# Kernel optimization log

Measured on AMD Instinct MI355X. Metric: run time of the kernel, lower is better.

Reference implementation:

```python
import jax, jax.numpy as jnp
import numpy as np

DIM = 2048
NUM_HEADS = 16
HEAD_DIM = DIM // NUM_HEADS
SCALE = 1.0 / float(np.sqrt(HEAD_DIM))


def setup_inputs() -> dict:
    key = jax.random.key(0)
    ks = jax.random.split(key, 7)
    B, L = 2, 2048
    x = jax.random.normal(ks[0], (B, L, DIM), dtype=jnp.float32)
    s = 1.0 / np.sqrt(DIM)
    # nn.Linear stores weight as [out, in]; y = x @ W.T + b
    Wq = jax.random.uniform(ks[1], (DIM, DIM), jnp.float32, -s, s)
    bq = jax.random.uniform(ks[2], (DIM,), jnp.float32, -s, s)
    Wk = jax.random.uniform(ks[3], (DIM, DIM), jnp.float32, -s, s)
    bk = jax.random.uniform(ks[4], (DIM,), jnp.float32, -s, s)
    Wv = jax.random.uniform(ks[5], (DIM, DIM), jnp.float32, -s, s)
    bv = jax.random.uniform(ks[6], (DIM,), jnp.float32, -s, s)
    return {"x": x, "Wq": Wq, "bq": bq, "Wk": Wk, "bk": bk, "Wv": Wv, "bv": bv}


def _attn(x, Wq, bq, Wk, bk, Wv, bv):
    B, L, D = x.shape
    H, Hd = NUM_HEADS, HEAD_DIM
    # projections: x @ W.T + b, then split heads -> [B, H, L, Hd]
    q = (x @ Wq.T + bq).reshape(B, L, H, Hd).transpose(0, 2, 1, 3)
    k = (x @ Wk.T + bk).reshape(B, L, H, Hd).transpose(0, 2, 1, 3)
    v = (x @ Wv.T + bv).reshape(B, L, H, Hd).transpose(0, 2, 1, 3)
    scores = jnp.einsum("bhqd,bhkd->bhqk", q, k) * SCALE  # [B,H,L,L]
    attn = jax.nn.softmax(scores, axis=-1)
    out = jnp.einsum("bhqk,bhkd->bhqd", attn, v)
    return out.transpose(0, 2, 1, 3).reshape(B, L, D)


def reference(x, Wq, bq, Wk, bk, Wv, bv):
    return _attn(x, Wq, bq, Wk, bk, Wv, bv)
```

## Files before the change

### kernel.cpp

```cpp
#include <hip/hip_runtime.h>
#include <stdint.h>

typedef unsigned short u16;
typedef __attribute__((ext_vector_type(8))) short short8;
typedef __attribute__((ext_vector_type(16))) float f32x16;

#define ATTN_SCALE 0.08838834764831845f

__device__ __forceinline__ u16 f2bf(float f) {
  union { float f; uint32_t u; } a; a.f = f;
  return (u16)((a.u + 0x7fffu + ((a.u >> 16) & 1u)) >> 16);
}

__device__ __forceinline__ void async16(const u16* g, u16* lds) {
  __builtin_amdgcn_global_load_lds(
      (const __attribute__((address_space(1))) void*)g,
      (__attribute__((address_space(3))) void*)lds, 16, 0, 0);
}

__global__ void cvt_kernel(const float* __restrict__ src, u16* __restrict__ dst, int n8) {
  int i = blockIdx.x * 256 + threadIdx.x;
  if (i >= n8) return;
  const float4* s4 = (const float4*)src;
  float4 a = s4[2 * i], c = s4[2 * i + 1];
  union { u16 h[8]; uint4 v; } o;
  o.h[0] = f2bf(a.x); o.h[1] = f2bf(a.y); o.h[2] = f2bf(a.z); o.h[3] = f2bf(a.w);
  o.h[4] = f2bf(c.x); o.h[5] = f2bf(c.y); o.h[6] = f2bf(c.z); o.h[7] = f2bf(c.w);
  ((uint4*)dst)[i] = o.v;
}

__global__ void cvtw_kernel(const float* __restrict__ w0, const float* __restrict__ w1,
                            const float* __restrict__ w2, u16* __restrict__ dst) {
  int z = blockIdx.y;
  const float* src = (z == 0) ? w0 : (z == 1) ? w1 : w2;
  int i = blockIdx.x * 256 + threadIdx.x;
  const float4* s4 = (const float4*)src;
  float4 a = s4[2 * i], c = s4[2 * i + 1];
  union { u16 h[8]; uint4 v; } o;
  o.h[0] = f2bf(a.x); o.h[1] = f2bf(a.y); o.h[2] = f2bf(a.z); o.h[3] = f2bf(a.w);
  o.h[4] = f2bf(c.x); o.h[5] = f2bf(c.y); o.h[6] = f2bf(c.z); o.h[7] = f2bf(c.w);
  ((uint4*)(dst + (size_t)z * 4194304))[i] = o.v;
}

__global__ __launch_bounds__(256, 4) void qkv_gemm(
    const u16* __restrict__ xb, const u16* __restrict__ Wb,
    const float* __restrict__ bq, const float* __restrict__ bk, const float* __restrict__ bv,
    u16* __restrict__ qkv) {
  __shared__ __align__(16) u16 As[2][128 * 32];
  __shared__ __align__(16) u16 Bs[2][128 * 32];
  const int z = blockIdx.z;
  const int n0 = blockIdx.x * 128, m0 = blockIdx.y * 128;
  const u16* Bw = Wb + (size_t)z * (2048u * 2048u);
  const float* bias = (z == 0) ? bq : (z == 1) ? bk : bv;
  u16* dst = qkv + (size_t)z * 8388608u;
  const int t = threadIdx.x, wave = t >> 6, lane = t & 63;
  const int wm = wave >> 1, wn = wave & 1, l31 = lane & 31, h = lane >> 5;

  int soff[2], goff[2];
#pragma unroll
  for (int p = 0; p < 2; ++p) {
    const int s = p * 256 + wave * 64 + lane;
    const int R = s >> 4, j = s & 15, u = j ^ (R & 15);
    const int m = R * 4 + (u >> 2), c = u & 3;
    soff[p] = s * 8;
    goff[p] = m * 2048 + c * 8;
  }
  int fr16[2][2], fR15[2][2];
  const int q4 = (l31 & 3) * 4;
#pragma unroll
  for (int i = 0; i < 2; ++i) {
    const int mA = wm * 64 + i * 32 + l31, mB = wn * 64 + i * 32 + l31;
    fr16[0][i] = (mA >> 2) * 16; fR15[0][i] = (mA >> 2) & 15;
    fr16[1][i] = (mB >> 2) * 16; fR15[1][i] = (mB >> 2) & 15;
  }

  f32x16 acc[2][2];
#pragma unroll
  for (int i = 0; i < 2; ++i)
#pragma unroll
    for (int j = 0; j < 2; ++j)
#pragma unroll
      for (int r = 0; r < 16; ++r) acc[i][j][r] = 0.f;

  const u16* Abase = xb + (size_t)m0 * 2048;
  const u16* Bbase = Bw + (size_t)n0 * 2048;

#pragma unroll 1
  for (int n = 0; n < 64; ++n) {
    if (n == 0) {
#pragma unroll
      for (int p = 0; p < 2; ++p) {
        async16(Abase + goff[p], &As[0][soff[p]]);
        async16(Bbase + goff[p], &Bs[0][soff[p]]);
      }
    }
    __syncthreads();
    const int cur = n & 1;
    if (n + 1 < 64) {
      const int k1 = (n + 1) * 32;
#pragma unroll
      for (int p = 0; p < 2; ++p) {
        async16(Abase + goff[p] + k1, &As[cur ^ 1][soff[p]]);
        async16(Bbase + goff[p] + k1, &Bs[cur ^ 1][soff[p]]);
      }
    }
#pragma unroll
    for (int ks = 0; ks < 2; ++ks) {
      const int c = ks * 2 + h;
      short8 af[2], bf[2];
#pragma unroll
      for (int i = 0; i < 2; ++i) {
        af[i] = *(const short8*)&As[cur][(fr16[0][i] + ((q4 + c) ^ fR15[0][i])) * 8];
        bf[i] = *(const short8*)&Bs[cur][(fr16[1][i] + ((q4 + c) ^ fR15[1][i])) * 8];
      }
#pragma unroll
      for (int i = 0; i < 2; ++i)
#pragma unroll
        for (int j = 0; j < 2; ++j)
          acc[i][j] = __builtin_amdgcn_mfma_f32_32x32x16_bf16(af[i], bf[j], acc[i][j], 0, 0, 0);
    }
  }

#pragma unroll
  for (int j = 0; j < 2; ++j) {
    const int col = n0 + wn * 64 + j * 32 + l31;
    const float bb_ = bias[col];
    const int hh = col >> 7, hd = col & 127;
#pragma unroll
    for (int i = 0; i < 2; ++i) {
#pragma unroll
      for (int g = 0; g < 4; ++g) {
        const int lbase = m0 + wm * 64 + i * 32 + 8 * g + 4 * h;
        const int bb = lbase >> 11, l0 = lbase & 2047;
        if (z == 2) {
          union { u16 q[4]; uint2 d; } pk;
#pragma unroll
          for (int rr = 0; rr < 4; ++rr) pk.q[rr] = f2bf(acc[i][j][4 * g + rr] + bb_);
          *(uint2*)&dst[((size_t)(bb * 16 + hh) * 128 + hd) * 2048 + l0] = pk.d;
        } else {
#pragma unroll
          for (int rr = 0; rr < 4; ++rr)
            dst[((size_t)(bb * 16 + hh) * 2048 + (l0 + rr)) * 128 + hd] =
                f2bf(acc[i][j][4 * g + rr] + bb_);
        }
      }
    }
  }
}

__global__ __launch_bounds__(256, 3) void attn_kernel(
    const u16* __restrict__ Qg,
    const u16* __restrict__ Kg,
    const u16* __restrict__ Vtg,
    float* __restrict__ out) {
  __shared__ __align__(16) u16 Ks[64 * 128];
  __shared__ __align__(16) u16 Vs[128 * 64];
  const int bh = blockIdx.y, q0 = blockIdx.x * 128;
  const int t = threadIdx.x, wave = t >> 6, lane = t & 63;
  const int l31 = lane & 31, h = lane >> 5;
  const u16* Qp = Qg + (size_t)bh * 262144;
  const u16* Kp = Kg + (size_t)bh * 262144;
  const u16* Vp = Vtg + (size_t)bh * 262144;
  const int b = bh >> 4, hd = bh & 15;
  const int qrow = q0 + wave * 32 + l31;

  short8 qf[8];
#pragma unroll
  for (int s = 0; s < 8; ++s)
    qf[s] = *(const short8*)&Qp[(size_t)qrow * 128 + s * 16 + h * 8];

  int kOff[4], kSlot[4], vOff[4], vSlot[4];
#pragma unroll
  for (int p = 0; p < 4; ++p) {
    const int s = p * 256 + wave * 64 + lane;
    const int rk = s >> 4, gk = (s & 15) ^ (rk & 15);
    kSlot[p] = s * 8; kOff[p] = rk * 128 + gk * 8;
    const int rv = s >> 3, gv = (s & 7) ^ (rv & 7);
    vSlot[p] = s * 8; vOff[p] = rv * 2048 + gv * 8;
  }

  f32x16 oac[4];
#pragma unroll
  for (int dt = 0; dt < 4; ++dt)
#pragma unroll
    for (int r = 0; r < 16; ++r) oac[dt][r] = 0.f;
  float den = 0.f;

#pragma unroll 1
  for (int kt = 0; kt < 32; ++kt) {
    const int k0 = kt * 64;
    __syncthreads();
#pragma unroll
    for (int p = 0; p < 4; ++p) async16(Kp + (size_t)k0 * 128 + kOff[p], &Ks[kSlot[p]]);
#pragma unroll
    for (int p = 0; p < 4; ++p) async16(Vp + (size_t)k0 + vOff[p], &Vs[vSlot[p]]);
    __syncthreads();

#pragma unroll
    for (int T = 0; T < 2; ++T) {
      const int krow = T * 32 + l31;
      f32x16 sc;
#pragma unroll
      for (int r = 0; r < 16; ++r) sc[r] = 0.f;
#pragma unroll
      for (int s = 0; s < 8; ++s) {
        const short8 kf = *(const short8*)&Ks[(krow * 16 + ((2 * s + h) ^ (krow & 15))) * 8];
        sc = __builtin_amdgcn_mfma_f32_32x32x16_bf16(kf, qf[s], sc, 0, 0, 0);
      }
      uint32_t pp[8];
#pragma unroll
      for (int i = 0; i < 8; ++i) {
        const float e0 = __expf(fminf(sc[2 * i] * ATTN_SCALE, 80.f));
        const float e1 = __expf(fminf(sc[2 * i + 1] * ATTN_SCALE, 80.f));
        den += e0 + e1;
        union { float f; uint32_t u; } u0, u1; u0.f = e0; u1.f = e1;
        pp[i] = ((u1.u + 0x8000u) & 0xffff0000u) | ((u0.u + 0x8000u) >> 16);
      }
      uint32_t x[8];
#pragma unroll
      for (int i = 0; i < 8; ++i) x[i] = __shfl_xor(pp[i], 32, 64);
#pragma unroll
      for (int ks = 0; ks < 2; ++ks) {
        const int o0 = ks * 4;
        union { uint32_t u[4]; short8 s8; } bfp;
        bfp.u[0] = h ? x[o0 + 2] : pp[o0 + 0];
        bfp.u[1] = h ? x[o0 + 3] : pp[o0 + 1];
        bfp.u[2] = h ? pp[o0 + 2] : x[o0 + 0];
        bfp.u[3] = h ? pp[o0 + 3] : x[o0 + 1];
        const int gk = T * 4 + ks * 2 + h;
#pragma unroll
        for (int dt = 0; dt < 4; ++dt) {
          const int vrow = dt * 32 + l31;
          const short8 vf = *(const short8*)&Vs[(vrow * 8 + (gk ^ (vrow & 7))) * 8];
          oac[dt] = __builtin_amdgcn_mfma_f32_32x32x16_bf16(vf, bfp.s8, oac[dt], 0, 0, 0);
        }
      }
    }
  }

  den += __shfl_xor(den, 32, 64);
  const float inv = 1.f / den;
#pragma unroll
  for (int dt = 0; dt < 4; ++dt) {
#pragma unroll
    for (int g4 = 0; g4 < 4; ++g4) {
      float4 o;
      o.x = oac[dt][4 * g4 + 0] * inv;
      o.y = oac[dt][4 * g4 + 1] * inv;
      o.z = oac[dt][4 * g4 + 2] * inv;
      o.w = oac[dt][4 * g4 + 3] * inv;
      const int d = dt * 32 + g4 * 8 + h * 4;
      *(float4*)&out[((size_t)(b * 2048 + qrow)) * 2048 + hd * 128 + d] = o;
    }
  }
}

extern "C" void kernel_launch(void* const* d_in, const int* in_sizes, int n_in,
                              void* d_out, int out_size, void* d_ws, size_t ws_size,
                              hipStream_t stream) {
  const float* x  = (const float*)d_in[0];
  const float* Wq = (const float*)d_in[1];
  const float* bq = (const float*)d_in[2];
  const float* Wk = (const float*)d_in[3];
  const float* bk = (const float*)d_in[4];
  const float* Wv = (const float*)d_in[5];
  const float* bv = (const float*)d_in[6];
  float* out = (float*)d_out;
  if (ws_size < 92274688u) return;

  u16* xb  = (u16*)d_ws;
  u16* Wb  = xb + 8388608;
  u16* qkv = Wb + 12582912;

  cvt_kernel<<<4096, 256, 0, stream>>>(x, xb, 1048576);
  cvtw_kernel<<<dim3(2048, 3), 256, 0, stream>>>(Wq, Wk, Wv, Wb);
  qkv_gemm<<<dim3(16, 32, 3), 256, 0, stream>>>(xb, Wb, bq, bk, bv, qkv);
  attn_kernel<<<dim3(16, 32), 256, 0, stream>>>(qkv, qkv + 8388608, qkv + 16777216, out);
}
```

Before: 350.8 us.

## Load K/V fragments directly from global memory and remap block order for L2 reuse

The attention kernel drops the LDS staging of K and V tiles and the two block-wide barriers per tile. Each wave now loads its MFMA K and V fragments straight from global memory through the cache. The block index is also remapped so consecutive workgroups are spread across (b,h) groups, to improve L2/MALL locality across XCDs. This removes synchronisation and LDS traffic, but each wave now reads K/V from global memory itself (4 waves re-read the same data), which relies on cache hits and lowers the occupancy hint from 3 to 2.

```diff
diff --git a/kernel.cpp b/kernel.cpp
--- a/kernel.cpp
+++ b/kernel.cpp
@@ -148,14 +148,14 @@
   }
 }
 
-__global__ __launch_bounds__(256, 3) void attn_kernel(
+__global__ __launch_bounds__(256, 2) void attn_kernel(
     const u16* __restrict__ Qg,
     const u16* __restrict__ Kg,
     const u16* __restrict__ Vtg,
     float* __restrict__ out) {
-  __shared__ __align__(16) u16 Ks[64 * 128];
-  __shared__ __align__(16) u16 Vs[128 * 64];
-  const int bh = blockIdx.y, q0 = blockIdx.x * 128;
+  const int s_lin = blockIdx.y * 16 + blockIdx.x;
+  const int w = (s_lin & 7) * 64 + (s_lin >> 3);
+  const int bh = w >> 4, q0 = (w & 15) * 128;
   const int t = threadIdx.x, wave = t >> 6, lane = t & 63;
   const int l31 = lane & 31, h = lane >> 5;
   const u16* Qp = Qg + (size_t)bh * 262144;
@@ -169,15 +169,8 @@
   for (int s = 0; s < 8; ++s)
     qf[s] = *(const short8*)&Qp[(size_t)qrow * 128 + s * 16 + h * 8];
 
-  int kOff[4], kSlot[4], vOff[4], vSlot[4];
-#pragma unroll
-  for (int p = 0; p < 4; ++p) {
-    const int s = p * 256 + wave * 64 + lane;
-    const int rk = s >> 4, gk = (s & 15) ^ (rk & 15);
-    kSlot[p] = s * 8; kOff[p] = rk * 128 + gk * 8;
-    const int rv = s >> 3, gv = (s & 7) ^ (rv & 7);
-    vSlot[p] = s * 8; vOff[p] = rv * 2048 + gv * 8;
-  }
+  const u16* Kl = Kp + (size_t)l31 * 128 + h * 8;
+  const u16* Vl = Vp + (size_t)l31 * 2048 + h * 8;
 
   f32x16 oac[4];
 #pragma unroll
@@ -189,24 +182,20 @@
 #pragma unroll 1
   for (int kt = 0; kt < 32; ++kt) {
     const int k0 = kt * 64;
-    __syncthreads();
-#pragma unroll
-    for (int p = 0; p < 4; ++p) async16(Kp + (size_t)k0 * 128 + kOff[p], &Ks[kSlot[p]]);
-#pragma unroll
-    for (int p = 0; p < 4; ++p) async16(Vp + (size_t)k0 + vOff[p], &Vs[vSlot[p]]);
-    __syncthreads();
-
 #pragma unroll
     for (int T = 0; T < 2; ++T) {
-      const int krow = T * 32 + l31;
+      const u16* Kt_ = Kl + (size_t)(k0 + T * 32) * 128;
+      short8 kf[8];
+#pragma unroll
+      for (int s = 0; s < 8; ++s)
+        kf[s] = *(const short8*)&Kt_[s * 16];
       f32x16 sc;
 #pragma unroll
       for (int r = 0; r < 16; ++r) sc[r] = 0.f;
 #pragma unroll
-      for (int s = 0; s < 8; ++s) {
-        const short8 kf = *(const short8*)&Ks[(krow * 16 + ((2 * s + h) ^ (krow & 15))) * 8];
-        sc = __builtin_amdgcn_mfma_f32_32x32x16_bf16(kf, qf[s], sc, 0, 0, 0);
-      }
+      for (int s = 0; s < 8; ++s)
+        sc = __builtin_amdgcn_mfma_f32_32x32x16_bf16(kf[s], qf[s], sc, 0, 0, 0);
+
       uint32_t pp[8];
 #pragma unroll
       for (int i = 0; i < 8; ++i) {
@@ -227,11 +216,10 @@
         bfp.u[1] = h ? x[o0 + 3] : pp[o0 + 1];
         bfp.u[2] = h ? pp[o0 + 2] : x[o0 + 0];
         bfp.u[3] = h ? pp[o0 + 3] : x[o0 + 1];
-        const int gk = T * 4 + ks * 2 + h;
+        const int vcol = k0 + T * 32 + ks * 16;
 #pragma unroll
         for (int dt = 0; dt < 4; ++dt) {
-          const int vrow = dt * 32 + l31;
-          const short8 vf = *(const short8*)&Vs[(vrow * 8 + (gk ^ (vrow & 7))) * 8];
+          const short8 vf = *(const short8*)&Vl[(size_t)dt * 65536 + vcol];
           oac[dt] = __builtin_amdgcn_mfma_f32_32x32x16_bf16(vf, bfp.s8, oac[dt], 0, 0, 0);
         }
       }
```

Measured after the change: 513.6 us. 1.46x slower.
